# Optimization experiments

Measured on AMD Instinct MI355X. Metric: run time of the kernel, lower is better.

The kernel has to match this reference:

```python
import jax, jax.numpy as jnp
import numpy as np

B, N, E = 16, 10000, 320000
C_IN, C_OUT, K = 32, 64, 3
C = C_IN + C_OUT          # 96, channels into each diffusion conv
L = 2 * K - 1             # 5 Chebyshev terms (bidirectional, remove_ln=False)


def setup_inputs() -> dict:
    key = jax.random.key(0)
    ks = jax.random.split(key, 8)
    x = jax.random.normal(ks[0], (B, N, C_IN), dtype=jnp.float32)
    hidden_state = jax.random.normal(ks[1], (B, N, C_OUT), dtype=jnp.float32)
    edge_index = jax.random.randint(ks[2], (2, E), 0, N, dtype=jnp.int64)
    edge_weight = jax.random.uniform(ks[3], (E,), dtype=jnp.float32)
    # xavier-uniform style scale for params
    s_ru = float(np.sqrt(6.0 / (L * C + 2 * C_OUT)))
    s_c = float(np.sqrt(6.0 / (L * C + C_OUT)))
    ru_param = jax.random.uniform(ks[4], (L * C, 2 * C_OUT), minval=-s_ru, maxval=s_ru, dtype=jnp.float32)
    ru_bias = jnp.zeros((2 * C_OUT,), dtype=jnp.float32)
    c_param = jax.random.uniform(ks[5], (L * C, C_OUT), minval=-s_c, maxval=s_c, dtype=jnp.float32)
    c_bias = jnp.zeros((C_OUT,), dtype=jnp.float32)
    return {"x": x, "hidden_state": hidden_state, "edge_index": edge_index,
            "edge_weight": edge_weight, "ru_param": ru_param, "ru_bias": ru_bias,
            "c_param": c_param, "c_bias": c_bias}


def _propagate(h, src, dst, w, num_nodes):
    # gather x_j at src, weight, scatter-add at dst: out[i] = sum_{e: dst=i} w_e * h[src_e]
    return jax.ops.segment_sum(h[src] * w[:, None], dst, num_segments=num_nodes)


def _cheb_conv(x, src, dst, wf, wb, param, bias, k):
    # x: [B, N, C] -> [N, B*C] as in torch transpose(0,1).view(N, B*C)
    b, n, c = x.shape
    xt = jnp.transpose(x, (1, 0, 2)).reshape(n, b * c)
    x0f = xt
    x0b = xt
    x1f = _propagate(xt, src, dst, wf, n)
    x1b = _propagate(xt, dst, src, wb, n)
    outs = [xt, x1f, x1b]
    for _ in range(2, k):
        x2f = 2.0 * _propagate(x1f, src, dst, wf, n) - x0f
        outs.append(x2f)
        x0f, x1f = x1f, x2f
        x2b = 2.0 * _propagate(x1b, dst, src, wb, n) - x0b
        outs.append(x2b)
        x0b, x1b = x1b, x2b
    out = jnp.stack(outs, axis=2)            # [N, B*C, L]
    out = out.reshape(n * b, -1)             # [N*B, C*L] (row-major matches torch view)
    out = out @ param                        # [N*B, out_channels]
    out = jnp.transpose(out.reshape(n, b, -1), (1, 0, 2))  # [B, N, out]
    return out + bias


def reference(x, hidden_state, edge_index, edge_weight, ru_param, ru_bias, c_param, c_bias):
    src, dst = edge_index[0], edge_index[1]
    n = x.shape[1]
    deg_f = jax.ops.segment_sum(edge_weight, src, num_segments=n)
    wf = edge_weight / deg_f[src]            # forward-diffusion normalized weights
    deg_b = jax.ops.segment_sum(edge_weight, dst, num_segments=n)
    wb = edge_weight / deg_b[dst]            # reverse-diffusion normalized weights

    x_and_state = jnp.concatenate([x, hidden_state], axis=2)
    ru = jax.nn.sigmoid(_cheb_conv(x_and_state, src, dst, wf, wb, ru_param, ru_bias, K))
    r = ru[:, :, :C_OUT]
    u = ru[:, :, C_OUT:]
    xrh = jnp.concatenate([x, r * hidden_state], axis=-1)
    # original applies tanh twice
    c = jnp.tanh(jnp.tanh(_cheb_conv(xrh, src, dst, wf, wb, c_param, c_bias, K)))
    return u * hidden_state + (1.0 - u) * c
```

## Files before the change

kernel.cpp:

```cpp
#include <hip/hip_runtime.h>
#include <stdint.h>
#include <stddef.h>

#define Bn    16
#define Nn    10000
#define En    320000
#define CIN   32
#define COUTn 64
#define CCn   96
#define WROWU 768
#define RHU   512
#define MROWS 160000

typedef __attribute__((ext_vector_type(8))) short short8;
typedef __attribute__((ext_vector_type(4))) float f32x4;
typedef __attribute__((ext_vector_type(2))) float f32x2;
typedef __attribute__((ext_vector_type(4))) unsigned int uint4v;

__device__ __forceinline__ float bflo(unsigned int p) { return __uint_as_float(p << 16); }
__device__ __forceinline__ float bfhi(unsigned int p) { return __uint_as_float(p & 0xffff0000u); }
__device__ __forceinline__ float bf2f(unsigned short u) { return __uint_as_float(((unsigned int)u) << 16); }
__device__ __forceinline__ unsigned int f2bfbits(float f) {
  unsigned int x = __float_as_uint(f);
  return (x + 0x7fffu + ((x >> 16) & 1u)) >> 16;
}
__device__ __forceinline__ unsigned int pack2(float lo, float hi) {
  return f2bfbits(lo) | (f2bfbits(hi) << 16);
}

__global__ void detect_idx(const int* __restrict__ idx, int* __restrict__ flag) {
  if (threadIdx.x == 0 && blockIdx.x == 0) {
    int is64 = 1;
    for (int i = 1; i < 128; i += 2) {
      if (idx[i] != 0) { is64 = 0; break; }
    }
    flag[0] = is64;
  }
}

__device__ __forceinline__ int gidx(const int* __restrict__ p, int i, int is64) {
  return is64 ? p[2 * (long long)i] : p[i];
}

__global__ void deg_cnt_kernel(const int* __restrict__ idx, const float* __restrict__ w,
                               float* __restrict__ deg_f, float* __restrict__ deg_b,
                               int* __restrict__ cnt_f, int* __restrict__ cnt_b,
                               const int* __restrict__ flag) {
  int e = blockIdx.x * 256 + threadIdx.x;
  int is64 = flag[0];
  if (e < En) {
    int s = gidx(idx, e, is64);
    int d = gidx(idx, En + e, is64);
    float we = w[e];
    atomicAdd(&deg_f[s], we);
    atomicAdd(&deg_b[d], we);
    atomicAdd(&cnt_f[d], 1);
    atomicAdd(&cnt_b[s], 1);
  }
}

__global__ void exscan_two(const int* __restrict__ cnt_f, const int* __restrict__ cnt_b,
                           int* __restrict__ rp_f, int* __restrict__ rp_b,
                           int* __restrict__ cur_f, int* __restrict__ cur_b, int n) {
  const int* cnt = (blockIdx.x == 0) ? cnt_f : cnt_b;
  int* rp  = (blockIdx.x == 0) ? rp_f  : rp_b;
  int* cur = (blockIdx.x == 0) ? cur_f : cur_b;
  __shared__ int sh[256];
  int t = threadIdx.x;
  int running = 0;
  for (int base = 0; base < n; base += 256) {
    int v = (base + t < n) ? cnt[base + t] : 0;
    sh[t] = v;
    __syncthreads();
    for (int off = 1; off < 256; off <<= 1) {
      int x = (t >= off) ? sh[t - off] : 0;
      __syncthreads();
      sh[t] += x;
      __syncthreads();
    }
    int excl = sh[t] - v;
    if (base + t < n) { rp[base + t] = running + excl; cur[base + t] = running + excl; }
    int total = sh[255];
    __syncthreads();
    running += total;
  }
  if (t == 0) rp[n] = running;
}

__global__ void fill_csr(const int* __restrict__ idx, const float* __restrict__ w,
                         const float* __restrict__ deg_f, const float* __restrict__ deg_b,
                         int* __restrict__ cur_f, int* __restrict__ cur_b,
                         uint2* __restrict__ cwf, uint2* __restrict__ cwb,
                         const int* __restrict__ flag) {
  int e = blockIdx.x * 256 + threadIdx.x;
  int is64 = flag[0];
  if (e < En) {
    int s = gidx(idx, e, is64);
    int d = gidx(idx, En + e, is64);
    float we = w[e];
    int pf = atomicAdd(&cur_f[d], 1);
    cwf[pf] = make_uint2((unsigned int)s, __float_as_uint(we / deg_f[s]));
    int pb = atomicAdd(&cur_b[s], 1);
    cwb[pb] = make_uint2((unsigned int)d, __float_as_uint(we / deg_b[d]));
  }
}

__global__ void build_wt(const float* __restrict__ ru_p, const float* __restrict__ c_p,
                         unsigned short* __restrict__ Wt1, unsigned short* __restrict__ Wt2) {
  int i = blockIdx.x * 256 + threadIdx.x;
  if (i < 128 * 480) {
    int n = i / 480, k = i % 480;
    int t = k / 96, kk = k % 96;
    float v;
    if (t == 0) v = ru_p[(kk * 5 + 0) * 128 + n] - ru_p[(kk * 5 + 3) * 128 + n] - ru_p[(kk * 5 + 4) * 128 + n];
    else        v = ru_p[(kk * 5 + t) * 128 + n];
    Wt1[i] = (unsigned short)f2bfbits(v);
  }
  if (i < 64 * 480) {
    int n = i / 480, k = i % 480;
    int t = k / 96, kk = k % 96;
    float v;
    if (t == 0) v = c_p[(kk * 5 + 0) * 64 + n] - c_p[(kk * 5 + 3) * 64 + n] - c_p[(kk * 5 + 4) * 64 + n];
    else        v = c_p[(kk * 5 + t) * 64 + n];
    Wt2[i] = (unsigned short)f2bfbits(v);
  }
}

__global__ void build_x0_ru(const float* __restrict__ x, const float* __restrict__ h,
                            unsigned int* __restrict__ X0) {
  long long p = (long long)blockIdx.x * 256 + threadIdx.x;
  int node = (int)(p / WROWU);
  int rem = (int)(p % WROWU);
  int b = rem / 48;
  int ci = (rem % 48) * 2;
  float lo, hi;
  if (ci < CIN) {
    const float* s = x + ((size_t)b * Nn + node) * CIN + ci;
    lo = s[0]; hi = s[1];
  } else {
    const float* s = h + ((size_t)b * Nn + node) * COUTn + (ci - CIN);
    lo = s[0]; hi = s[1];
  }
  X0[p] = pack2(lo, hi);
}

template<int RU4, int ACT, int EPW>
__device__ __forceinline__ void prop_rowX(const uint4v* __restrict__ in,
                                          uint4v* __restrict__ out,
                                          const int* __restrict__ rp,
                                          const uint2* __restrict__ cw,
                                          int row, int slice, int lane, float alpha) {
  constexpr int GSZ = 64 / EPW;
  constexpr unsigned RB = (unsigned)RU4 * 16u;
  int grp = (EPW == 2) ? (lane >> 5) : (lane >> 4);
  int lg = lane & (GSZ - 1);
  int lgc = (lg < ACT) ? lg : 0;
  unsigned laneByte = (unsigned)(slice * ACT + lgc) * 16u;
  const char* __restrict__ inB = (const char*)in;
  int jb = __builtin_amdgcn_readfirstlane(rp[row]);
  int je = __builtin_amdgcn_readfirstlane(rp[row + 1]);
  int len = je - jb;

  f32x2 a0 = {0.f, 0.f}, a1 = {0.f, 0.f}, a2 = {0.f, 0.f}, a3 = {0.f, 0.f};

  constexpr int STEP = 4 * EPW;
  int i = jb;
  int eM = jb + (len / STEP) * STEP;
  for (; i < eM; i += STEP) {
    #pragma unroll
    for (int k = 0; k < 4; ++k) {
      unsigned int col; float w;
      {
        uint2 e0 = cw[i + k * EPW + 0];
        uint2 e1 = cw[i + k * EPW + 1];
        col = (grp & 1) ? e1.x : e0.x;
        w = __uint_as_float((grp & 1) ? e1.y : e0.y);
        if (EPW == 4) {
          uint2 e2 = cw[i + k * EPW + 2];
          uint2 e3 = cw[i + k * EPW + 3];
          unsigned int colB = (grp & 1) ? e3.x : e2.x;
          float wB = __uint_as_float((grp & 1) ? e3.y : e2.y);
          col = (grp & 2) ? colB : col;
          w = (grp & 2) ? wB : w;
        }
      }
      unsigned off = __umul24(col, RB) + laneByte;
      uint4v q = *(const uint4v*)(inB + off);
      f32x2 wv = {w, w};
      f32x2 v0 = {bflo(q.x), bfhi(q.x)};
      f32x2 v1 = {bflo(q.y), bfhi(q.y)};
      f32x2 v2 = {bflo(q.z), bfhi(q.z)};
      f32x2 v3 = {bflo(q.w), bfhi(q.w)};
      a0 += wv * v0; a1 += wv * v1; a2 += wv * v2; a3 += wv * v3;
    }
  }
  for (; i < je; i += EPW) {
    unsigned int col; float w;
    {
      uint2 e0 = cw[i + 0];
      uint2 e1 = cw[(i + 1 < je) ? i + 1 : i];
      col = (grp & 1) ? e1.x : e0.x;
      w = __uint_as_float((grp & 1) ? e1.y : e0.y);
      if (EPW == 4) {
        uint2 e2 = cw[(i + 2 < je) ? i + 2 : i];
        uint2 e3 = cw[(i + 3 < je) ? i + 3 : i];
        unsigned int colB = (grp & 1) ? e3.x : e2.x;
        float wB = __uint_as_float((grp & 1) ? e3.y : e2.y);
        col = (grp & 2) ? colB : col;
        w = (grp & 2) ? wB : w;
      }
    }
    if (i + grp >= je) w = 0.f;
    unsigned off = __umul24(col, RB) + laneByte;
    uint4v q = *(const uint4v*)(inB + off);
    f32x2 wv = {w, w};
    f32x2 v0 = {bflo(q.x), bfhi(q.x)};
    f32x2 v1 = {bflo(q.y), bfhi(q.y)};
    f32x2 v2 = {bflo(q.z), bfhi(q.z)};
    f32x2 v3 = {bflo(q.w), bfhi(q.w)};
    a0 += wv * v0; a1 += wv * v1; a2 += wv * v2; a3 += wv * v3;
  }

  #pragma unroll
  for (int k = 0; k < 2; ++k) {
    float* pa = (k == 0) ? (float*)&a0 : (float*)&a2;
  }
  {
    float* aa = (float*)&a0;
  }
  if (EPW == 4) {
    a0.x += __shfl_xor(a0.x, 16); a0.y += __shfl_xor(a0.y, 16);
    a1.x += __shfl_xor(a1.x, 16); a1.y += __shfl_xor(a1.y, 16);
    a2.x += __shfl_xor(a2.x, 16); a2.y += __shfl_xor(a2.y, 16);
    a3.x += __shfl_xor(a3.x, 16); a3.y += __shfl_xor(a3.y, 16);
  }
  a0.x += __shfl_xor(a0.x, 32); a0.y += __shfl_xor(a0.y, 32);
  a1.x += __shfl_xor(a1.x, 32); a1.y += __shfl_xor(a1.y, 32);
  a2.x += __shfl_xor(a2.x, 32); a2.y += __shfl_xor(a2.y, 32);
  a3.x += __shfl_xor(a3.x, 32); a3.y += __shfl_xor(a3.y, 32);

  if (grp == 0 && lg < ACT) {
    uint4v o;
    o.x = pack2(alpha * a0.x, alpha * a0.y);
    o.y = pack2(alpha * a1.x, alpha * a1.y);
    o.z = pack2(alpha * a2.x, alpha * a2.y);
    o.w = pack2(alpha * a3.x, alpha * a3.y);
    out[(size_t)row * RU4 + slice * ACT + lg] = o;
  }
}

template<int RU4, int ACT, int EPW>
__launch_bounds__(256)
__global__ void prop_dualX(const uint4v* __restrict__ in,
                           uint4v* __restrict__ outF, uint4v* __restrict__ outB,
                           const int* __restrict__ rp_f, const uint2* __restrict__ cwf,
                           const int* __restrict__ rp_b, const uint2* __restrict__ cwb) {
  int lane = threadIdx.x & 63;
  int wave = threadIdx.x >> 6;
  int slice = blockIdx.x & 7;
  int row = ((blockIdx.x >> 3) << 2) + wave;
  prop_rowX<RU4, ACT, EPW>(in, outF, rp_f, cwf, row, slice, lane, 1.f);
  prop_rowX<RU4, ACT, EPW>(in, outB, rp_b, cwb, row, slice, lane, 1.f);
}

template<int RU4, int ACT, int EPW>
__launch_bounds__(256)
__global__ void prop_ckX(const uint4v* __restrict__ in, uint4v* __restrict__ out,
                         const int* __restrict__ rp, const uint2* __restrict__ cw,
                         float alpha) {
  int lane = threadIdx.x & 63;
  int wave = threadIdx.x >> 6;
  int slice = blockIdx.x & 7;
  int row = ((blockIdx.x >> 3) << 2) + wave;
  prop_rowX<RU4, ACT, EPW>(in, out, rp, cw, row, slice, lane, alpha);
}

struct Msrc {
  const uint4* xs[5];
  const uint4* rh[5];
};

template<int NT, int MODE>
__launch_bounds__(256)
__global__ void gemm_mfma(Msrc g, int nterms, int t0,
                          const unsigned short* __restrict__ Wt,
                          const float* __restrict__ bias,
                          float* __restrict__ outp,
                          unsigned short* __restrict__ rh0_s,
                          unsigned short* __restrict__ U_out,
                          const unsigned short* __restrict__ U_in,
                          const float* __restrict__ hglob) {
  constexpr int NJ = NT / 16;
  __shared__ __align__(16) unsigned short As[128][104];
  __shared__ __align__(16) unsigned short Bs[NT][104];

  int m0 = blockIdx.x * 128;
  int tid = threadIdx.x;
  int wave = tid >> 6;
  int lane = tid & 63;
  int quad = lane >> 4;
  int lm = lane & 15;
  int wm = wave * 32;
  int nodeBase = m0 >> 4;

  f32x4 acc[2][NJ];
  #pragma unroll
  for (int i = 0; i < 2; ++i)
    #pragma unroll
    for (int j = 0; j < NJ; ++j) acc[i][j] = (f32x4){0.f, 0.f, 0.f, 0.f};

  for (int t = 0; t < nterms; ++t) {
    const uint4* xs4 = g.xs[t];
    const uint4* rh4 = g.rh[t];
    if (rh4 == nullptr) {
      const uint4* src = xs4 + (size_t)m0 * 12;
      #pragma unroll
      for (int it = 0; it < 6; ++it) {
        int q = tid + it * 256;
        uint4 v = src[q];
        int row = q / 12, slot = q % 12;
        *(uint4*)&As[row][slot * 8] = v;
      }
    } else {
      #pragma unroll
      for (int it = 0; it < 6; ++it) {
        int q = tid + it * 256;
        int row = q / 12, slot = q % 12;
        int node = nodeBase + (row >> 4);
        int b = row & 15;
        uint4 v; int ci0;
        if (slot < 4) { v = xs4[(size_t)node * 192 + b * 12 + slot]; ci0 = slot * 8; }
        else          { v = rh4[(size_t)node * 128 + b * 8 + (slot - 4)]; ci0 = 32 + (slot - 4) * 8; }
        *(uint4*)&As[row][ci0] = v;
      }
    }
    for (int q = tid; q < NT * 12; q += 256) {
      int n = q / 12, slot = q % 12;
      uint4 v = *(const uint4*)(Wt + (size_t)n * 480 + (t0 + t) * 96 + slot * 8);
      *(uint4*)&Bs[n][slot * 8] = v;
    }
    __syncthreads();

    #pragma unroll
    for (int k32 = 0; k32 < 3; ++k32) {
      int kb = k32 * 32 + quad * 8;
      short8 a0 = *(const short8*)&As[wm + lm][kb];
      short8 a1 = *(const short8*)&As[wm + 16 + lm][kb];
      #pragma unroll
      for (int j = 0; j < NJ; ++j) {
        short8 bf = *(const short8*)&Bs[j * 16 + lm][kb];
        acc[0][j] = __builtin_amdgcn_mfma_f32_16x16x32_bf16(a0, bf, acc[0][j], 0, 0, 0);
        acc[1][j] = __builtin_amdgcn_mfma_f32_16x16x32_bf16(a1, bf, acc[1][j], 0, 0, 0);
      }
    }
    __syncthreads();
  }

  #pragma unroll
  for (int i = 0; i < 2; ++i) {
    #pragma unroll
    for (int j = 0; j < NJ; ++j) {
      int col = j * 16 + lm;
      #pragma unroll
      for (int r = 0; r < 4; ++r) {
        int row = m0 + wm + i * 16 + quad * 4 + r;
        int node = row >> 4, b = row & 15;
        float v = acc[i][j][r];
        if (MODE == 0) {
          float s = 1.f / (1.f + expf(-(bias[col] + v)));
          if (col < COUTn) {
            float hv = hglob[((size_t)b * Nn + node) * COUTn + col];
            rh0_s[(size_t)row * 64 + col] = (unsigned short)f2bfbits(s * hv);
          } else {
            U_out[(size_t)row * 64 + (col - COUTn)] = (unsigned short)f2bfbits(s);
          }
        } else if (MODE == 1) {
          outp[((size_t)b * Nn + node) * COUTn + col] = bias[col] + v;
        } else {
          size_t oa = ((size_t)b * Nn + node) * COUTn + col;
          float cp = outp[oa] + v;
          float c = tanhf(tanhf(cp));
          float u = bf2f(U_in[(size_t)row * 64 + col]);
          outp[oa] = u * hglob[oa] + (1.f - u) * c;
        }
      }
    }
  }
}

extern "C" void kernel_launch(void* const* d_in, const int* in_sizes, int n_in,
                              void* d_out, int out_size, void* d_ws, size_t ws_size,
                              hipStream_t stream) {
  const float* x   = (const float*)d_in[0];
  const float* h   = (const float*)d_in[1];
  const int*   idx = (const int*)d_in[2];
  const float* ew  = (const float*)d_in[3];
  const float* ru_param = (const float*)d_in[4];
  const float* ru_bias  = (const float*)d_in[5];
  const float* c_param  = (const float*)d_in[6];
  const float* c_bias   = (const float*)d_in[7];
  float* outp = (float*)d_out;
  (void)in_sizes; (void)n_in; (void)out_size; (void)ws_size;

  char* ws = (char*)d_ws;
  size_t off = 0;
  auto alloc = [&](size_t bytes) -> char* {
    char* p = ws + off;
    off += (bytes + 255) & ~(size_t)255;
    return p;
  };

  float* deg_f = (float*)alloc(40960);
  float* deg_b = (float*)alloc(40960);
  int*   cnt_f = (int*)alloc(40960);
  int*   cnt_b = (int*)alloc(40960);
  int*   rp_f  = (int*)alloc((Nn + 1) * sizeof(int));
  int*   rp_b  = (int*)alloc((Nn + 1) * sizeof(int));
  int*   cur_f = (int*)alloc(Nn * sizeof(int));
  int*   cur_b = (int*)alloc(Nn * sizeof(int));
  int*   flag  = (int*)alloc(256);
  uint2* cwf   = (uint2*)alloc((size_t)En * 8);
  uint2* cwb   = (uint2*)alloc((size_t)En * 8);
  unsigned short* Wt1 = (unsigned short*)alloc(128 * 480 * 2);
  unsigned short* Wt2 = (unsigned short*)alloc(64 * 480 * 2);

  unsigned int* A0   = (unsigned int*)alloc((size_t)Nn * WROWU * 4);
  unsigned int* T1f  = (unsigned int*)alloc((size_t)Nn * WROWU * 4);
  unsigned int* T1b  = (unsigned int*)alloc((size_t)Nn * WROWU * 4);
  unsigned int* T2f  = (unsigned int*)alloc((size_t)Nn * WROWU * 4);
  unsigned int* T2b  = (unsigned int*)alloc((size_t)Nn * WROWU * 4);
  unsigned int* rh0  = (unsigned int*)alloc((size_t)Nn * RHU * 4);
  unsigned int* rh1f = (unsigned int*)alloc((size_t)Nn * RHU * 4);
  unsigned int* rh1b = (unsigned int*)alloc((size_t)Nn * RHU * 4);
  unsigned int* Ubuf = (unsigned int*)alloc((size_t)Nn * RHU * 4);

  hipMemsetAsync(ws, 0, 4 * 40960, stream);
  detect_idx<<<1, 64, 0, stream>>>(idx, flag);
  deg_cnt_kernel<<<En / 256, 256, 0, stream>>>(idx, ew, deg_f, deg_b, cnt_f, cnt_b, flag);
  exscan_two<<<2, 256, 0, stream>>>(cnt_f, cnt_b, rp_f, rp_b, cur_f, cur_b, Nn);
  fill_csr<<<En / 256, 256, 0, stream>>>(idx, ew, deg_f, deg_b, cur_f, cur_b,
                                         cwf, cwb, flag);
  build_wt<<<240, 256, 0, stream>>>(ru_param, c_param, Wt1, Wt2);

  const int gBuild = Nn * WROWU / 256;
  const int gP = (Nn / 4) * 8;

  build_x0_ru<<<gBuild, 256, 0, stream>>>(x, h, A0);
  prop_dualX<192, 24, 2><<<gP, 256, 0, stream>>>(
      (const uint4v*)A0, (uint4v*)T1f, (uint4v*)T1b, rp_f, cwf, rp_b, cwb);
  prop_ckX<192, 24, 2><<<gP, 256, 0, stream>>>(
      (const uint4v*)T1f, (uint4v*)T2f, rp_f, cwf, 2.f);
  prop_ckX<192, 24, 2><<<gP, 256, 0, stream>>>(
      (const uint4v*)T1b, (uint4v*)T2b, rp_b, cwb, 2.f);

  Msrc g1;
  g1.xs[0] = (const uint4*)A0;  g1.rh[0] = nullptr;
  g1.xs[1] = (const uint4*)T1f; g1.rh[1] = nullptr;
  g1.xs[2] = (const uint4*)T1b; g1.rh[2] = nullptr;
  g1.xs[3] = (const uint4*)T2f; g1.rh[3] = nullptr;
  g1.xs[4] = (const uint4*)T2b; g1.rh[4] = nullptr;
  gemm_mfma<128, 0><<<MROWS / 128, 256, 0, stream>>>(
      g1, 5, 0, Wt1, ru_bias, nullptr,
      (unsigned short*)rh0, (unsigned short*)Ubuf, nullptr, h);

  prop_dualX<128, 16, 4><<<gP, 256, 0, stream>>>(
      (const uint4v*)rh0, (uint4v*)rh1f, (uint4v*)rh1b, rp_f, cwf, rp_b, cwb);

  Msrc g2a;
  g2a.xs[0] = (const uint4*)A0;  g2a.rh[0] = (const uint4*)rh0;
  g2a.xs[1] = (const uint4*)T1f; g2a.rh[1] = (const uint4*)rh1f;
  g2a.xs[2] = (const uint4*)T1b; g2a.rh[2] = (const uint4*)rh1b;
  g2a.xs[3] = nullptr; g2a.rh[3] = nullptr;
  g2a.xs[4] = nullptr; g2a.rh[4] = nullptr;
  gemm_mfma<64, 1><<<MROWS / 128, 256, 0, stream>>>(
      g2a, 3, 0, Wt2, c_bias, outp, nullptr, nullptr, nullptr, nullptr);

  prop_ckX<128, 16, 4><<<gP, 256, 0, stream>>>(
      (const uint4v*)rh1f, (uint4v*)rh0, rp_f, cwf, 2.f);
  prop_ckX<128, 16, 4><<<gP, 256, 0, stream>>>(
      (const uint4v*)rh1b, (uint4v*)rh1f, rp_b, cwb, 2.f);

  Msrc g2b;
  g2b.xs[0] = (const uint4*)T2f; g2b.rh[0] = (const uint4*)rh0;
  g2b.xs[1] = (const uint4*)T2b; g2b.rh[1] = (const uint4*)rh1f;
  g2b.xs[2] = nullptr; g2b.rh[2] = nullptr;
  g2b.xs[3] = nullptr; g2b.rh[3] = nullptr;
  g2b.xs[4] = nullptr; g2b.rh[4] = nullptr;
  gemm_mfma<64, 2><<<MROWS / 128, 256, 0, stream>>>(
      g2b, 2, 3, Wt2, c_bias, outp, nullptr, nullptr,
      (const unsigned short*)Ubuf, h);
}
```

Baseline: 922.7 us.

## Fuse second-stage GEMM with Chebyshev propagations, parallelize scan and setup kernels

Runs the first c-conv GEMM and the two second-order propagations of r*h in one launch, with block-index ranges dispatching to the GEMM body or to forward/backward propagation rows. Outputs go to new buffers so the GEMM's inputs are no longer overwritten, which removes launch serialization and lets the compute-bound GEMM overlap the memory-bound gathers. It also replaces the serial chunked exclusive scan with a per-thread segmented scan, merges weight and X0 construction into one launch, and uses a wave ballot for index-width detection. The fused kernel needs extra workspace and only runs when it fits, otherwise the old path is used; the heterogeneous blocks may limit occupancy because the GEMM's shared memory is allocated for every block.

```diff
diff --git a/kernel.cpp b/kernel.cpp
--- a/kernel.cpp
+++ b/kernel.cpp
@@ -11,6 +11,7 @@
 #define WROWU 768
 #define RHU   512
 #define MROWS 160000
+#define GX0   (Nn * WROWU / 256)
 
 typedef __attribute__((ext_vector_type(8))) short short8;
 typedef __attribute__((ext_vector_type(4))) float f32x4;
@@ -29,13 +30,10 @@
 }
 
 __global__ void detect_idx(const int* __restrict__ idx, int* __restrict__ flag) {
-  if (threadIdx.x == 0 && blockIdx.x == 0) {
-    int is64 = 1;
-    for (int i = 1; i < 128; i += 2) {
-      if (idx[i] != 0) { is64 = 0; break; }
-    }
-    flag[0] = is64;
-  }
+  int t = threadIdx.x;
+  int v = idx[1 + 2 * t];
+  unsigned long long bal = __ballot(v != 0);
+  if (t == 0) flag[0] = (bal == 0ULL) ? 1 : 0;
 }
 
 __device__ __forceinline__ int gidx(const int* __restrict__ p, int i, int is64) {
@@ -67,24 +65,24 @@
   int* cur = (blockIdx.x == 0) ? cur_f : cur_b;
   __shared__ int sh[256];
   int t = threadIdx.x;
-  int running = 0;
-  for (int base = 0; base < n; base += 256) {
-    int v = (base + t < n) ? cnt[base + t] : 0;
-    sh[t] = v;
+  int CH = (n + 255) / 256;
+  int s0 = t * CH;
+  int s1 = s0 + CH; if (s1 > n) s1 = n;
+  int s = 0;
+  for (int i = s0; i < s1; ++i) s += cnt[i];
+  sh[t] = s;
+  __syncthreads();
+  for (int off = 1; off < 256; off <<= 1) {
+    int x = (t >= off) ? sh[t - off] : 0;
     __syncthreads();
-    for (int off = 1; off < 256; off <<= 1) {
-      int x = (t >= off) ? sh[t - off] : 0;
-      __syncthreads();
-      sh[t] += x;
-      __syncthreads();
-    }
-    int excl = sh[t] - v;
-    if (base + t < n) { rp[base + t] = running + excl; cur[base + t] = running + excl; }
-    int total = sh[255];
+    sh[t] += x;
     __syncthreads();
-    running += total;
-  }
-  if (t == 0) rp[n] = running;
+  }
+  int run = sh[t] - s;
+  for (int i = s0; i < s1; ++i) {
+    rp[i] = run; cur[i] = run; run += cnt[i];
+  }
+  if (t == 255) rp[n] = sh[255];
 }
 
 __global__ void fill_csr(const int* __restrict__ idx, const float* __restrict__ w,
@@ -105,43 +103,44 @@
   }
 }
 
-__global__ void build_wt(const float* __restrict__ ru_p, const float* __restrict__ c_p,
-                         unsigned short* __restrict__ Wt1, unsigned short* __restrict__ Wt2) {
-  int i = blockIdx.x * 256 + threadIdx.x;
-  if (i < 128 * 480) {
-    int n = i / 480, k = i % 480;
-    int t = k / 96, kk = k % 96;
-    float v;
-    if (t == 0) v = ru_p[(kk * 5 + 0) * 128 + n] - ru_p[(kk * 5 + 3) * 128 + n] - ru_p[(kk * 5 + 4) * 128 + n];
-    else        v = ru_p[(kk * 5 + t) * 128 + n];
-    Wt1[i] = (unsigned short)f2bfbits(v);
-  }
-  if (i < 64 * 480) {
-    int n = i / 480, k = i % 480;
-    int t = k / 96, kk = k % 96;
-    float v;
-    if (t == 0) v = c_p[(kk * 5 + 0) * 64 + n] - c_p[(kk * 5 + 3) * 64 + n] - c_p[(kk * 5 + 4) * 64 + n];
-    else        v = c_p[(kk * 5 + t) * 64 + n];
-    Wt2[i] = (unsigned short)f2bfbits(v);
-  }
-}
-
-__global__ void build_x0_ru(const float* __restrict__ x, const float* __restrict__ h,
-                            unsigned int* __restrict__ X0) {
-  long long p = (long long)blockIdx.x * 256 + threadIdx.x;
-  int node = (int)(p / WROWU);
-  int rem = (int)(p % WROWU);
-  int b = rem / 48;
-  int ci = (rem % 48) * 2;
-  float lo, hi;
-  if (ci < CIN) {
-    const float* s = x + ((size_t)b * Nn + node) * CIN + ci;
-    lo = s[0]; hi = s[1];
+__global__ void build_x0_wt(const float* __restrict__ x, const float* __restrict__ h,
+                            unsigned int* __restrict__ X0,
+                            const float* __restrict__ ru_p, const float* __restrict__ c_p,
+                            unsigned short* __restrict__ Wt1, unsigned short* __restrict__ Wt2) {
+  if (blockIdx.x < GX0) {
+    long long p = (long long)blockIdx.x * 256 + threadIdx.x;
+    int node = (int)(p / WROWU);
+    int rem = (int)(p % WROWU);
+    int b = rem / 48;
+    int ci = (rem % 48) * 2;
+    float lo, hi;
+    if (ci < CIN) {
+      const float* s = x + ((size_t)b * Nn + node) * CIN + ci;
+      lo = s[0]; hi = s[1];
+    } else {
+      const float* s = h + ((size_t)b * Nn + node) * COUTn + (ci - CIN);
+      lo = s[0]; hi = s[1];
+    }
+    X0[p] = pack2(lo, hi);
   } else {
-    const float* s = h + ((size_t)b * Nn + node) * COUTn + (ci - CIN);
-    lo = s[0]; hi = s[1];
-  }
-  X0[p] = pack2(lo, hi);
+    int i = (blockIdx.x - GX0) * 256 + threadIdx.x;
+    if (i < 128 * 480) {
+      int n = i / 480, k = i % 480;
+      int t = k / 96, kk = k % 96;
+      float v;
+      if (t == 0) v = ru_p[(kk * 5 + 0) * 128 + n] - ru_p[(kk * 5 + 3) * 128 + n] - ru_p[(kk * 5 + 4) * 128 + n];
+      else        v = ru_p[(kk * 5 + t) * 128 + n];
+      Wt1[i] = (unsigned short)f2bfbits(v);
+    }
+    if (i < 64 * 480) {
+      int n = i / 480, k = i % 480;
+      int t = k / 96, kk = k % 96;
+      float v;
+      if (t == 0) v = c_p[(kk * 5 + 0) * 64 + n] - c_p[(kk * 5 + 3) * 64 + n] - c_p[(kk * 5 + 4) * 64 + n];
+      else        v = c_p[(kk * 5 + t) * 64 + n];
+      Wt2[i] = (unsigned short)f2bfbits(v);
+    }
+  }
 }
 
 template<int RU4, int ACT, int EPW>
@@ -221,13 +220,6 @@
     a0 += wv * v0; a1 += wv * v1; a2 += wv * v2; a3 += wv * v3;
   }
 
-  #pragma unroll
-  for (int k = 0; k < 2; ++k) {
-    float* pa = (k == 0) ? (float*)&a0 : (float*)&a2;
-  }
-  {
-    float* aa = (float*)&a0;
-  }
   if (EPW == 4) {
     a0.x += __shfl_xor(a0.x, 16); a0.y += __shfl_xor(a0.y, 16);
     a1.x += __shfl_xor(a1.x, 16); a1.y += __shfl_xor(a1.y, 16);
@@ -281,8 +273,7 @@
 };
 
 template<int NT, int MODE>
-__launch_bounds__(256)
-__global__ void gemm_mfma(Msrc g, int nterms, int t0,
+__device__ __forceinline__ void gemm_body(int blk, Msrc g, int nterms, int t0,
                           const unsigned short* __restrict__ Wt,
                           const float* __restrict__ bias,
                           float* __restrict__ outp,
@@ -294,7 +285,7 @@
   __shared__ __align__(16) unsigned short As[128][104];
   __shared__ __align__(16) unsigned short Bs[NT][104];
 
-  int m0 = blockIdx.x * 128;
+  int m0 = blk * 128;
   int tid = threadIdx.x;
   int wave = tid >> 6;
   int lane = tid & 63;
@@ -388,6 +379,45 @@
   }
 }
 
+template<int NT, int MODE>
+__launch_bounds__(256)
+__global__ void gemm_mfma(Msrc g, int nterms, int t0,
+                          const unsigned short* __restrict__ Wt,
+                          const float* __restrict__ bias,
+                          float* __restrict__ outp,
+                          unsigned short* __restrict__ rh0_s,
+                          unsigned short* __restrict__ U_out,
+                          const unsigned short* __restrict__ U_in,
+                          const float* __restrict__ hglob) {
+  gemm_body<NT, MODE>(blockIdx.x, g, nterms, t0, Wt, bias, outp, rh0_s, U_out, U_in, hglob);
+}
+
+__launch_bounds__(256)
+__global__ void fused_g2a(Msrc g,
+                          const unsigned short* __restrict__ Wt,
+                          const float* __restrict__ bias,
+                          float* __restrict__ outp,
+                          const uint4v* __restrict__ inF, uint4v* __restrict__ outF,
+                          const int* __restrict__ rp_f, const uint2* __restrict__ cwf,
+                          const uint4v* __restrict__ inB, uint4v* __restrict__ outB,
+                          const int* __restrict__ rp_b, const uint2* __restrict__ cwb) {
+  int b = blockIdx.x;
+  if (b < 1256) {
+    if (b < 1250)
+      gemm_body<64, 1>(b, g, 3, 0, Wt, bias, outp, nullptr, nullptr, nullptr, nullptr);
+    return;
+  }
+  int lane = threadIdx.x & 63;
+  int wave = threadIdx.x >> 6;
+  if (b < 21256) {
+    int b2 = b - 1256;
+    prop_rowX<128, 16, 4>(inF, outF, rp_f, cwf, ((b2 >> 3) << 2) + wave, b2 & 7, lane, 2.f);
+  } else {
+    int b2 = b - 21256;
+    prop_rowX<128, 16, 4>(inB, outB, rp_b, cwb, ((b2 >> 3) << 2) + wave, b2 & 7, lane, 2.f);
+  }
+}
+
 extern "C" void kernel_launch(void* const* d_in, const int* in_sizes, int n_in,
                               void* d_out, int out_size, void* d_ws, size_t ws_size,
                               hipStream_t stream) {
@@ -400,7 +430,7 @@
   const float* c_param  = (const float*)d_in[6];
   const float* c_bias   = (const float*)d_in[7];
   float* outp = (float*)d_out;
-  (void)in_sizes; (void)n_in; (void)out_size; (void)ws_size;
+  (void)in_sizes; (void)n_in; (void)out_size;
 
   char* ws = (char*)d_ws;
   size_t off = 0;
@@ -433,6 +463,9 @@
   unsigned int* rh1f = (unsigned int*)alloc((size_t)Nn * RHU * 4);
   unsigned int* rh1b = (unsigned int*)alloc((size_t)Nn * RHU * 4);
   unsigned int* Ubuf = (unsigned int*)alloc((size_t)Nn * RHU * 4);
+  unsigned int* rh2fN = (unsigned int*)alloc((size_t)Nn * RHU * 4);
+  unsigned int* rh2bN = (unsigned int*)alloc((size_t)Nn * RHU * 4);
+  bool bigws = (off <= ws_size);
 
   hipMemsetAsync(ws, 0, 4 * 40960, stream);
   detect_idx<<<1, 64, 0, stream>>>(idx, flag);
@@ -440,12 +473,10 @@
   exscan_two<<<2, 256, 0, stream>>>(cnt_f, cnt_b, rp_f, rp_b, cur_f, cur_b, Nn);
   fill_csr<<<En / 256, 256, 0, stream>>>(idx, ew, deg_f, deg_b, cur_f, cur_b,
                                          cwf, cwb, flag);
-  build_wt<<<240, 256, 0, stream>>>(ru_param, c_param, Wt1, Wt2);
-
-  const int gBuild = Nn * WROWU / 256;
+  build_x0_wt<<<GX0 + 240, 256, 0, stream>>>(x, h, A0, ru_param, c_param, Wt1, Wt2);
+
   const int gP = (Nn / 4) * 8;
 
-  build_x0_ru<<<gBuild, 256, 0, stream>>>(x, h, A0);
   prop_dualX<192, 24, 2><<<gP, 256, 0, stream>>>(
       (const uint4v*)A0, (uint4v*)T1f, (uint4v*)T1b, rp_f, cwf, rp_b, cwb);
   prop_ckX<192, 24, 2><<<gP, 256, 0, stream>>>(
@@ -472,17 +503,30 @@
   g2a.xs[2] = (const uint4*)T1b; g2a.rh[2] = (const uint4*)rh1b;
   g2a.xs[3] = nullptr; g2a.rh[3] = nullptr;
   g2a.xs[4] = nullptr; g2a.rh[4] = nullptr;
-  gemm_mfma<64, 1><<<MROWS / 128, 256, 0, stream>>>(
-      g2a, 3, 0, Wt2, c_bias, outp, nullptr, nullptr, nullptr, nullptr);
-
-  prop_ckX<128, 16, 4><<<gP, 256, 0, stream>>>(
-      (const uint4v*)rh1f, (uint4v*)rh0, rp_f, cwf, 2.f);
-  prop_ckX<128, 16, 4><<<gP, 256, 0, stream>>>(
-      (const uint4v*)rh1b, (uint4v*)rh1f, rp_b, cwb, 2.f);
+
+  const uint4* g2b_rh0;
+  const uint4* g2b_rh1;
+  if (bigws) {
+    fused_g2a<<<41256, 256, 0, stream>>>(
+        g2a, Wt2, c_bias, outp,
+        (const uint4v*)rh1f, (uint4v*)rh2fN, rp_f, cwf,
+        (const uint4v*)rh1b, (uint4v*)rh2bN, rp_b, cwb);
+    g2b_rh0 = (const uint4*)rh2fN;
+    g2b_rh1 = (const uint4*)rh2bN;
+  } else {
+    gemm_mfma<64, 1><<<MROWS / 128, 256, 0, stream>>>(
+        g2a, 3, 0, Wt2, c_bias, outp, nullptr, nullptr, nullptr, nullptr);
+    prop_ckX<128, 16, 4><<<gP, 256, 0, stream>>>(
+        (const uint4v*)rh1f, (uint4v*)rh0, rp_f, cwf, 2.f);
+    prop_ckX<128, 16, 4><<<gP, 256, 0, stream>>>(
+        (const uint4v*)rh1b, (uint4v*)rh1f, rp_b, cwb, 2.f);
+    g2b_rh0 = (const uint4*)rh0;
+    g2b_rh1 = (const uint4*)rh1f;
+  }
 
   Msrc g2b;
-  g2b.xs[0] = (const uint4*)T2f; g2b.rh[0] = (const uint4*)rh0;
-  g2b.xs[1] = (const uint4*)T2b; g2b.rh[1] = (const uint4*)rh1f;
+  g2b.xs[0] = (const uint4*)T2f; g2b.rh[0] = g2b_rh0;
+  g2b.xs[1] = (const uint4*)T2b; g2b.rh[1] = g2b_rh1;
   g2b.xs[2] = nullptr; g2b.rh[2] = nullptr;
   g2b.xs[3] = nullptr; g2b.rh[3] = nullptr;
   g2b.xs[4] = nullptr; g2b.rh[4] = nullptr;
```

New measurement: 852.0 us. 1.08x faster.
